# Optimization experiments

Hardware: AMD Instinct MI355X
Metric: run time of the kernel (lower is better)

Reference implementation:

```python
import jax, jax.numpy as jnp
from jax import lax
import numpy as np

B, T, D, H, K = 16, 2048, 512, 512, 2

def setup_inputs() -> dict:
    key = jax.random.key(0)
    k1, k2, k3 = jax.random.split(key, 3)
    inputs = jax.random.normal(k1, (B, T, D), dtype=jnp.float32)
    conv_w = jax.random.normal(k2, (3 * H, D, K), dtype=jnp.float32) * (1.0 / np.sqrt(D * K))
    conv_b = jax.random.normal(k3, (3 * H,), dtype=jnp.float32) * 0.01
    return {"inputs": inputs, "conv_w": conv_w, "conv_b": conv_b}

def reference(inputs, conv_w, conv_b):
    # inputs: [B, T, D]; conv_w: [3H, D, K]; causal conv via left-pad K-1
    k = conv_w.shape[-1]
    h = conv_w.shape[0] // 3
    x = jnp.transpose(inputs, (0, 2, 1))                      # [B, D, T]
    x = jnp.pad(x, ((0, 0), (0, 0), (k - 1, 0)))              # left pad
    gates = lax.conv_general_dilated(
        x, conv_w, window_strides=(1,), padding='VALID',
        dimension_numbers=('NCH', 'OIH', 'NCH'))              # [B, 3H, T]
    gates = jnp.transpose(gates, (0, 2, 1)) + conv_b          # [B, T, 3H]
    Z, F, O = jnp.split(gates, 3, axis=2)
    Z = jnp.tanh(Z)
    F = jax.nn.sigmoid(F)
    O = jax.nn.sigmoid(O)

    # fo-pool: c_t = f_t * c_{t-1} + (1 - f_t) * z_t, c_{-1} = 0
    def step(c, zf):
        z, f = zf
        c_ = f * c + (1.0 - f) * z
        return c_, c_

    c0 = jnp.zeros((Z.shape[0], h), dtype=Z.dtype)
    _, C = lax.scan(step, c0, (jnp.swapaxes(Z, 0, 1), jnp.swapaxes(F, 0, 1)))
    C = jnp.swapaxes(C, 0, 1)                                 # [B, T, H]
    return C, O * C
```

## Files before the change

### kernel.cpp

```cpp
#include <hip/hip_runtime.h>


#define MTOT 32768
#define NTOT 1536
#define KTOT 1024
#define DCH  512
#define TLEN 2048
#define NB   16

#define LC2    64
#define NCH    32
#define CHAINS 8192

typedef __bf16 bf16x8 __attribute__((ext_vector_type(8)));
typedef float  f32x4  __attribute__((ext_vector_type(4)));

__device__ __forceinline__ unsigned short f2bf(float x) {
    unsigned u = __float_as_uint(x);
    u += 0x7FFFu + ((u >> 16) & 1u);
    return (unsigned short)(u >> 16);
}
__device__ __forceinline__ float bf2f(unsigned short h) {
    return __uint_as_float(((unsigned)h) << 16);
}
__device__ __forceinline__ float sigmoidf_(float x) {
    return 1.f / (1.f + __expf(-x));
}

__global__ __launch_bounds__(256) void make_A(const float* __restrict__ in,
                                              unsigned short* __restrict__ A) {
    size_t i = (size_t)blockIdx.x * 256 + threadIdx.x;
    size_t e = i * 8;
    size_t m = e >> 10;
    int    j = (int)(e & 1023);
    alignas(16) unsigned short h[8];
    if (((m & (TLEN - 1)) == 0) && (j < DCH)) {
#pragma unroll
        for (int r = 0; r < 8; ++r) h[r] = 0;
    } else {
        const float* src = in + ((long long)m - 1) * DCH + j;
        float4 a = *(const float4*)src;
        float4 b = *(const float4*)(src + 4);
        h[0] = f2bf(a.x); h[1] = f2bf(a.y); h[2] = f2bf(a.z); h[3] = f2bf(a.w);
        h[4] = f2bf(b.x); h[5] = f2bf(b.y); h[6] = f2bf(b.z); h[7] = f2bf(b.w);
    }
    *(int4*)(A + e) = *(const int4*)h;
}

__global__ __launch_bounds__(256) void make_B(const float* __restrict__ w,
                                              unsigned short* __restrict__ Bt) {
    int i = blockIdx.x * 256 + threadIdx.x;
    int o = i >> 9, d = i & 511;
    float w0 = w[(size_t)(o * 512 + d) * 2];
    float w1 = w[(size_t)(o * 512 + d) * 2 + 1];
    Bt[(size_t)o * 1024 + d]       = f2bf(w0);
    Bt[(size_t)o * 1024 + 512 + d] = f2bf(w1);
}

__global__ __launch_bounds__(256) void gemm_gates(const unsigned short* __restrict__ A,
                                                  const unsigned short* __restrict__ B,
                                                  const float* __restrict__ bias,
                                                  unsigned short* __restrict__ GT) {
    __shared__ int4 sA[512];
    __shared__ int4 sB[512];

    const int tid = threadIdx.x;
    const int bx0 = blockIdx.x;
    const int bx  = (bx0 & 7) * 384 + (bx0 >> 3);
    const int mT  = bx / 12, nT = bx % 12;
    const int m0  = mT * 128, n0 = nT * 128;

    const int mloc = tid >> 2;
    const int qsw  = (tid & 3) ^ ((mloc >> 1) & 3);
    const unsigned short* ga0 = A + (size_t)(m0 + mloc) * 1024 + qsw * 8;
    const unsigned short* ga1 = A + (size_t)(m0 + 64 + mloc) * 1024 + qsw * 8;
    const unsigned short* gb0 = B + (size_t)(n0 + mloc) * 1024 + qsw * 8;
    const unsigned short* gb1 = B + (size_t)(n0 + 64 + mloc) * 1024 + qsw * 8;

    char* la0 = (char*)sA + tid * 16;
    char* la1 = (char*)sA + 4096 + tid * 16;
    char* lb0 = (char*)sB + tid * 16;
    char* lb1 = (char*)sB + 4096 + tid * 16;

    const int lane = tid & 63;
    const int wv   = tid >> 6;
    const int wm   = (wv & 1) * 64, wn = (wv >> 1) * 64;
    const int lr   = lane & 15, lq = lane >> 4;

    int sAidx[4], sBidx[4];
#pragma unroll
    for (int i = 0; i < 4; ++i) {
        int mi = wm + 16 * i + lr;
        sAidx[i] = mi * 4 + (lq ^ ((mi >> 1) & 3));
        int ni = wn + 16 * i + lr;
        sBidx[i] = ni * 4 + (lq ^ ((ni >> 1) & 3));
    }

    f32x4 acc[4][4] = {};

    for (int kt = 0; kt < KTOT; kt += 32) {
        __builtin_amdgcn_global_load_lds(
            (__attribute__((address_space(1))) void*)(void*)ga0,
            (__attribute__((address_space(3))) void*)la0, 16, 0, 0);
        __builtin_amdgcn_global_load_lds(
            (__attribute__((address_space(1))) void*)(void*)ga1,
            (__attribute__((address_space(3))) void*)la1, 16, 0, 0);
        __builtin_amdgcn_global_load_lds(
            (__attribute__((address_space(1))) void*)(void*)gb0,
            (__attribute__((address_space(3))) void*)lb0, 16, 0, 0);
        __builtin_amdgcn_global_load_lds(
            (__attribute__((address_space(1))) void*)(void*)gb1,
            (__attribute__((address_space(3))) void*)lb1, 16, 0, 0);
        ga0 += 32; ga1 += 32; gb0 += 32; gb1 += 32;
        __syncthreads();

        bf16x8 af[4], bfr[4];
#pragma unroll
        for (int i = 0; i < 4; ++i) af[i]  = __builtin_bit_cast(bf16x8, sA[sAidx[i]]);
#pragma unroll
        for (int j = 0; j < 4; ++j) bfr[j] = __builtin_bit_cast(bf16x8, sB[sBidx[j]]);

#pragma unroll
        for (int i = 0; i < 4; ++i)
#pragma unroll
            for (int j = 0; j < 4; ++j)
                acc[i][j] = __builtin_amdgcn_mfma_f32_16x16x32_bf16(af[i], bfr[j],
                                                                    acc[i][j], 0, 0, 0);
        __syncthreads();
    }

#pragma unroll
    for (int j = 0; j < 4; ++j) {
        int gn = n0 + wn + 16 * j + lr;
        float bj = bias[gn];
#pragma unroll
        for (int i = 0; i < 4; ++i) {
            int rowb = m0 + wm + 16 * i + lq * 4;
            alignas(8) unsigned short pk[4];
#pragma unroll
            for (int r = 0; r < 4; ++r) pk[r] = f2bf(acc[i][j][r] + bj);
            *(int2*)(GT + (size_t)gn * MTOT + rowb) = *(const int2*)pk;
        }
    }
}

__global__ __launch_bounds__(256) void scan_part1(const unsigned short* __restrict__ GT,
                                                  float* __restrict__ Pws,
                                                  float* __restrict__ Cws) {
    const int tid   = threadIdx.x;
    const int h_loc = tid & 31;
    const int sc    = tid >> 5;
    const int bid   = blockIdx.x;
    const int tg    = bid & 3;
    const int hg    = (bid >> 2) & 15;
    const int b     = bid >> 6;
    const int h     = hg * 32 + h_loc;
    const int cg    = tg * 8 + sc;

    const size_t mbase = (size_t)b * TLEN + (size_t)cg * LC2;
    const unsigned short* gz = GT + (size_t)h * MTOT + mbase;
    const unsigned short* gf = GT + (size_t)(DCH + h) * MTOT + mbase;

    bf16x8 zv[8], fv[8];
#pragma unroll
    for (int q = 0; q < 8; ++q) zv[q] = *(const bf16x8*)(gz + q * 8);
#pragma unroll
    for (int q = 0; q < 8; ++q) fv[q] = *(const bf16x8*)(gf + q * 8);

    float P = 1.f, c = 0.f;
#pragma unroll
    for (int q = 0; q < 8; ++q)
#pragma unroll
        for (int r = 0; r < 8; ++r) {
            float f = sigmoidf_((float)fv[q][r]);
            float z = 2.f * sigmoidf_(2.f * (float)zv[q][r]) - 1.f;
            c = f * c + (1.f - f) * z;
            P *= f;
        }
    const int ch = b * DCH + h;
    Pws[(size_t)cg * CHAINS + ch] = P;
    Cws[(size_t)cg * CHAINS + ch] = c;
}

__global__ __launch_bounds__(256) void scan_part2(const float* __restrict__ Pws,
                                                  const float* __restrict__ Cws,
                                                  float* __restrict__ Iws) {
    const int ch = blockIdx.x * 256 + threadIdx.x;
    float Pv[NCH], Cv[NCH];
#pragma unroll
    for (int cg = 0; cg < NCH; ++cg) Pv[cg] = Pws[(size_t)cg * CHAINS + ch];
#pragma unroll
    for (int cg = 0; cg < NCH; ++cg) Cv[cg] = Cws[(size_t)cg * CHAINS + ch];
    float cc = 0.f;
#pragma unroll
    for (int cg = 0; cg < NCH; ++cg) {
        Iws[(size_t)cg * CHAINS + ch] = cc;
        cc = Pv[cg] * cc + Cv[cg];
    }
}

__global__ __launch_bounds__(256) void scan_part3(const unsigned short* __restrict__ GT,
                                                  const float* __restrict__ Iws,
                                                  float* __restrict__ out) {
    const int tid   = threadIdx.x;
    const int h_loc = tid & 31;
    const int sc    = tid >> 5;
    const int bid   = blockIdx.x;
    const int tg    = bid & 3;
    const int hg    = (bid >> 2) & 15;
    const int b     = bid >> 6;
    const int h     = hg * 32 + h_loc;
    const int cg    = tg * 8 + sc;

    const size_t mbase = (size_t)b * TLEN + (size_t)cg * LC2;
    const unsigned short* gz = GT + (size_t)h * MTOT + mbase;
    const unsigned short* gf = GT + (size_t)(DCH + h) * MTOT + mbase;
    const unsigned short* go = GT + (size_t)(2 * DCH + h) * MTOT + mbase;

    bf16x8 zv[8], fv[8], ov[8];
#pragma unroll
    for (int q = 0; q < 8; ++q) zv[q] = *(const bf16x8*)(gz + q * 8);
#pragma unroll
    for (int q = 0; q < 8; ++q) fv[q] = *(const bf16x8*)(gf + q * 8);
#pragma unroll
    for (int q = 0; q < 8; ++q) ov[q] = *(const bf16x8*)(go + q * 8);

    const int ch = b * DCH + h;
    float c = Iws[(size_t)cg * CHAINS + ch];

    const size_t BTH = (size_t)NB * TLEN * DCH;
    float* oC  = out + mbase * DCH + h;
    float* oOC = oC + BTH;
#pragma unroll
    for (int q = 0; q < 8; ++q)
#pragma unroll
        for (int r = 0; r < 8; ++r) {
            float f = sigmoidf_((float)fv[q][r]);
            float z = 2.f * sigmoidf_(2.f * (float)zv[q][r]) - 1.f;
            float o = sigmoidf_((float)ov[q][r]);
            c = f * c + (1.f - f) * z;
            __builtin_nontemporal_store(c,     oC  + (size_t)(q * 8 + r) * DCH);
            __builtin_nontemporal_store(o * c, oOC + (size_t)(q * 8 + r) * DCH);
        }
}

extern "C" void kernel_launch(void* const* d_in, const int* in_sizes, int n_in,
                              void* d_out, int out_size, void* d_ws, size_t ws_size,
                              hipStream_t stream) {
    const float* in   = (const float*)d_in[0];
    const float* w    = (const float*)d_in[1];
    const float* bias = (const float*)d_in[2];
    float* out = (float*)d_out;

    unsigned short* Abf = (unsigned short*)d_ws;
    unsigned short* Bbf = Abf + (size_t)MTOT * 1024;
    unsigned short* GT  = Bbf + (size_t)NTOT * 1024;

    float* Pws = (float*)d_ws;
    float* Cws = Pws + (size_t)NCH * CHAINS;
    float* Iws = Cws + (size_t)NCH * CHAINS;

    make_A<<<dim3(16384), dim3(256), 0, stream>>>(in, Abf);
    make_B<<<dim3(3072),  dim3(256), 0, stream>>>(w, Bbf);
    gemm_gates<<<dim3(3072), dim3(256), 0, stream>>>(Abf, Bbf, bias, GT);
    scan_part1<<<dim3(1024), dim3(256), 0, stream>>>(GT, Pws, Cws);
    scan_part2<<<dim3(CHAINS / 256), dim3(256), 0, stream>>>(Pws, Cws, Iws);
    scan_part3<<<dim3(1024), dim3(256), 0, stream>>>(GT, Iws, out);
}
```

Baseline: 418.6 us.

## Enlarge GEMM tile to 256x256 with 4-stage async LDS pipeline

Reworks the gates GEMM from 128x128 tiles with 256 threads and a single synchronous LDS buffer into 256x256 tiles with 512 threads and a 4-deep ring of LDS buffers. Global-to-LDS loads run three k-steps ahead and are gated by vmcnt waits, with setprio around the MFMA blocks. The aim is to hide memory latency and raise operand reuse per LDS load. In exchange it uses 128KB of LDS and 128 accumulator floats per thread, which limits occupancy to one block per CU and leaves only 768 blocks.

```diff
diff --git a/kernel.cpp b/kernel.cpp
--- a/kernel.cpp
+++ b/kernel.cpp
@@ -11,6 +11,9 @@
 #define LC2    64
 #define NCH    32
 #define CHAINS 8192
+
+#define GBK 32
+#define NKT (KTOT / GBK)
 
 typedef __bf16 bf16x8 __attribute__((ext_vector_type(8)));
 typedef float  f32x4  __attribute__((ext_vector_type(4)));
@@ -57,89 +60,113 @@
     Bt[(size_t)o * 1024 + 512 + d] = f2bf(w1);
 }
 
-__global__ __launch_bounds__(256) void gemm_gates(const unsigned short* __restrict__ A,
+__global__ __launch_bounds__(512) void gemm_gates(const unsigned short* __restrict__ A,
                                                   const unsigned short* __restrict__ B,
                                                   const float* __restrict__ bias,
                                                   unsigned short* __restrict__ GT) {
-    __shared__ int4 sA[512];
-    __shared__ int4 sB[512];
+    __shared__ int4 lds4[8192];
 
     const int tid = threadIdx.x;
     const int bx0 = blockIdx.x;
-    const int bx  = (bx0 & 7) * 384 + (bx0 >> 3);
-    const int mT  = bx / 12, nT = bx % 12;
-    const int m0  = mT * 128, n0 = nT * 128;
-
-    const int mloc = tid >> 2;
-    const int qsw  = (tid & 3) ^ ((mloc >> 1) & 3);
-    const unsigned short* ga0 = A + (size_t)(m0 + mloc) * 1024 + qsw * 8;
-    const unsigned short* ga1 = A + (size_t)(m0 + 64 + mloc) * 1024 + qsw * 8;
-    const unsigned short* gb0 = B + (size_t)(n0 + mloc) * 1024 + qsw * 8;
-    const unsigned short* gb1 = B + (size_t)(n0 + 64 + mloc) * 1024 + qsw * 8;
-
-    char* la0 = (char*)sA + tid * 16;
-    char* la1 = (char*)sA + 4096 + tid * 16;
-    char* lb0 = (char*)sB + tid * 16;
-    char* lb1 = (char*)sB + 4096 + tid * 16;
+    const int bx  = (bx0 & 7) * 96 + (bx0 >> 3);
+    const int mT  = bx / 6, nT = bx % 6;
+    const int m0  = mT * 256, n0 = nT * 256;
+
+    const int r0 = tid >> 2, q = tid & 3;
+    const int qs = q ^ ((r0 >> 1) & 3);
+    const unsigned short* ga0 = A + (size_t)(m0 + r0) * 1024 + qs * 8;
+    const unsigned short* ga1 = A + (size_t)(m0 + 128 + r0) * 1024 + qs * 8;
+    const unsigned short* gb0 = B + (size_t)(n0 + r0) * 1024 + qs * 8;
+    const unsigned short* gb1 = B + (size_t)(n0 + 128 + r0) * 1024 + qs * 8;
+    char* ldsc = (char*)lds4;
 
     const int lane = tid & 63;
     const int wv   = tid >> 6;
-    const int wm   = (wv & 1) * 64, wn = (wv >> 1) * 64;
+    const int wm   = wv >> 2, wn = wv & 3;
     const int lr   = lane & 15, lq = lane >> 4;
 
-    int sAidx[4], sBidx[4];
-#pragma unroll
-    for (int i = 0; i < 4; ++i) {
-        int mi = wm + 16 * i + lr;
-        sAidx[i] = mi * 4 + (lq ^ ((mi >> 1) & 3));
-        int ni = wn + 16 * i + lr;
-        sBidx[i] = ni * 4 + (lq ^ ((ni >> 1) & 3));
-    }
-
-    f32x4 acc[4][4] = {};
-
-    for (int kt = 0; kt < KTOT; kt += 32) {
-        __builtin_amdgcn_global_load_lds(
-            (__attribute__((address_space(1))) void*)(void*)ga0,
-            (__attribute__((address_space(3))) void*)la0, 16, 0, 0);
-        __builtin_amdgcn_global_load_lds(
-            (__attribute__((address_space(1))) void*)(void*)ga1,
-            (__attribute__((address_space(3))) void*)la1, 16, 0, 0);
-        __builtin_amdgcn_global_load_lds(
-            (__attribute__((address_space(1))) void*)(void*)gb0,
-            (__attribute__((address_space(3))) void*)lb0, 16, 0, 0);
-        __builtin_amdgcn_global_load_lds(
-            (__attribute__((address_space(1))) void*)(void*)gb1,
-            (__attribute__((address_space(3))) void*)lb1, 16, 0, 0);
-        ga0 += 32; ga1 += 32; gb0 += 32; gb1 += 32;
-        __syncthreads();
-
-        bf16x8 af[4], bfr[4];
-#pragma unroll
-        for (int i = 0; i < 4; ++i) af[i]  = __builtin_bit_cast(bf16x8, sA[sAidx[i]]);
-#pragma unroll
-        for (int j = 0; j < 4; ++j) bfr[j] = __builtin_bit_cast(bf16x8, sB[sBidx[j]]);
-
-#pragma unroll
-        for (int i = 0; i < 4; ++i)
-#pragma unroll
-            for (int j = 0; j < 4; ++j)
-                acc[i][j] = __builtin_amdgcn_mfma_f32_16x16x32_bf16(af[i], bfr[j],
-                                                                    acc[i][j], 0, 0, 0);
-        __syncthreads();
-    }
-
+    int aidx[2][4], bidx[4];
+#pragma unroll
+    for (int h = 0; h < 2; ++h)
+#pragma unroll
+        for (int i = 0; i < 4; ++i) {
+            int row = wm * 128 + h * 64 + i * 16 + lr;
+            aidx[h][i] = row * 4 + (lq ^ ((row >> 1) & 3));
+        }
 #pragma unroll
     for (int j = 0; j < 4; ++j) {
-        int gn = n0 + wn + 16 * j + lr;
+        int col = wn * 64 + j * 16 + lr;
+        bidx[j] = 1024 + col * 4 + (lq ^ ((col >> 1) & 3));
+    }
+
+    f32x4 acc[8][4] = {};
+
+#define GLL(SRC, DOFF) __builtin_amdgcn_global_load_lds( \
+        (__attribute__((address_space(1))) void*)(void*)(SRC), \
+        (__attribute__((address_space(3))) void*)(ldsc + (DOFF)), 16, 0, 0)
+
+#define STAGE_A(U) { const int bb_ = ((U) & 3) * 32768; \
+        GLL(ga0 + (size_t)(U) * GBK, bb_ + tid * 16); \
+        GLL(ga1 + (size_t)(U) * GBK, bb_ + 8192 + tid * 16); }
+#define STAGE_B(U) { const int bb_ = ((U) & 3) * 32768; \
+        GLL(gb0 + (size_t)(U) * GBK, bb_ + 16384 + tid * 16); \
+        GLL(gb1 + (size_t)(U) * GBK, bb_ + 24576 + tid * 16); }
+
+    STAGE_A(0); STAGE_B(0);
+    STAGE_A(1); STAGE_B(1);
+    STAGE_A(2); STAGE_B(2);
+
+#define TILE(T, VW, DO_STAGE) { \
+        asm volatile("s_waitcnt vmcnt(" VW ")" ::: "memory"); \
+        __builtin_amdgcn_s_barrier(); \
+        __builtin_amdgcn_sched_barrier(0); \
+        const int bufo = ((T) & 3) * 2048; \
+        bf16x8 bf[4], af[4]; \
+        _Pragma("unroll") \
+        for (int j = 0; j < 4; ++j) bf[j] = __builtin_bit_cast(bf16x8, lds4[bufo + bidx[j]]); \
+        _Pragma("unroll") \
+        for (int i = 0; i < 4; ++i) af[i] = __builtin_bit_cast(bf16x8, lds4[bufo + aidx[0][i]]); \
+        if (DO_STAGE) STAGE_A((T) + 3); \
+        __builtin_amdgcn_s_setprio(1); \
+        _Pragma("unroll") \
+        for (int i = 0; i < 4; ++i) \
+            _Pragma("unroll") \
+            for (int j = 0; j < 4; ++j) \
+                acc[i][j] = __builtin_amdgcn_mfma_f32_16x16x32_bf16(af[i], bf[j], acc[i][j], 0, 0, 0); \
+        __builtin_amdgcn_s_setprio(0); \
+        _Pragma("unroll") \
+        for (int i = 0; i < 4; ++i) af[i] = __builtin_bit_cast(bf16x8, lds4[bufo + aidx[1][i]]); \
+        if (DO_STAGE) STAGE_B((T) + 3); \
+        __builtin_amdgcn_s_setprio(1); \
+        _Pragma("unroll") \
+        for (int i = 0; i < 4; ++i) \
+            _Pragma("unroll") \
+            for (int j = 0; j < 4; ++j) \
+                acc[4 + i][j] = __builtin_amdgcn_mfma_f32_16x16x32_bf16(af[i], bf[j], acc[4 + i][j], 0, 0, 0); \
+        __builtin_amdgcn_s_setprio(0); }
+
+    for (int t = 0; t < NKT - 3; ++t)
+        TILE(t, "8", 1);
+    TILE(NKT - 3, "8", 0);
+    TILE(NKT - 2, "4", 0);
+    TILE(NKT - 1, "0", 0);
+
+#undef TILE
+#undef STAGE_A
+#undef STAGE_B
+#undef GLL
+
+#pragma unroll
+    for (int j = 0; j < 4; ++j) {
+        int gn = n0 + wn * 64 + j * 16 + lr;
         float bj = bias[gn];
 #pragma unroll
-        for (int i = 0; i < 4; ++i) {
-            int rowb = m0 + wm + 16 * i + lq * 4;
+        for (int i = 0; i < 8; ++i) {
+            int gm = m0 + wm * 128 + i * 16 + lq * 4;
             alignas(8) unsigned short pk[4];
 #pragma unroll
             for (int r = 0; r < 4; ++r) pk[r] = f2bf(acc[i][j][r] + bj);
-            *(int2*)(GT + (size_t)gn * MTOT + rowb) = *(const int2*)pk;
+            *(int2*)(GT + (size_t)gn * MTOT + gm) = *(const int2*)pk;
         }
     }
 }
@@ -262,7 +289,7 @@
 
     make_A<<<dim3(16384), dim3(256), 0, stream>>>(in, Abf);
     make_B<<<dim3(3072),  dim3(256), 0, stream>>>(w, Bbf);
-    gemm_gates<<<dim3(3072), dim3(256), 0, stream>>>(Abf, Bbf, bias, GT);
+    gemm_gates<<<dim3(768), dim3(512), 0, stream>>>(Abf, Bbf, bias, GT);
     scan_part1<<<dim3(1024), dim3(256), 0, stream>>>(GT, Pws, Cws);
     scan_part2<<<dim3(CHAINS / 256), dim3(256), 0, stream>>>(Pws, Cws, Iws);
     scan_part3<<<dim3(1024), dim3(256), 0, stream>>>(GT, Iws, out);
```

Measured after the change: 400.4 us. 1.05x faster.
